# Optimization experiments

Hardware: AMD Instinct MI355X
Metric: run time of the kernel (lower is better)

Reference implementation:

```python
import jax, jax.numpy as jnp
import numpy as np

QUERY_INDS = (0, 1, 2, 3)
HEADS = 8
HEAD_DIM = 64
SCALE = HEAD_DIM ** -0.5
DIM = 512
INNER = HEADS * HEAD_DIM  # 512


def setup_inputs() -> dict:
    key = jax.random.key(0)
    ks = jax.random.split(key, 6)
    B, N = 4, 2048
    x = jax.random.normal(ks[0], (B, N, DIM), dtype=jnp.float32)
    bias = jax.random.normal(ks[1], (B, HEADS, N, N), dtype=jnp.float32)
    # weights stored as (in, out); math-equivalent to torch Linear
    Wq = jax.random.normal(ks[2], (DIM, INNER), dtype=jnp.float32) * (DIM ** -0.5)
    Wkv = jax.random.normal(ks[3], (DIM, 2 * INNER), dtype=jnp.float32) * (DIM ** -0.5)
    Wo = jax.random.normal(ks[4], (INNER, DIM), dtype=jnp.float32) * (INNER ** -0.5)
    bo = jax.random.normal(ks[5], (DIM,), dtype=jnp.float32) * 0.01
    return {"x": x, "bias": bias, "Wq": Wq, "Wkv": Wkv, "Wo": Wo, "bo": bo}


def _split_heads(t):
    # (B, n, H*d) -> (B, H, n, d)
    B, n, _ = t.shape
    return t.reshape(B, n, HEADS, HEAD_DIM).transpose(0, 2, 1, 3)


def reference(x, bias, Wq, Wkv, Wo, bo):
    qi = jnp.array(QUERY_INDS)
    q = _split_heads(x[:, qi] @ Wq)          # (B, H, M, d), M = len(QUERY_INDS)
    kv = x @ Wkv                              # (B, N, 2*inner)
    k, v = jnp.split(kv, 2, axis=-1)
    k = _split_heads(k)                       # (B, H, N, d)
    v = _split_heads(v)                       # (B, H, N, d)
    dots = jnp.einsum('bhmd,bhnd->bhmn', q, k) * SCALE
    dots = dots + bias[:, :, qi]              # gather bias rows at query positions
    attn = jax.nn.softmax(dots, axis=-1)      # dropout=0 (eval)
    out = jnp.einsum('bhmn,bhnd->bhmd', attn, v)
    B, _, M, _ = out.shape
    out = out.transpose(0, 2, 1, 3).reshape(B, M, INNER)  # (B, M, H*d)
    return out @ Wo + bo
```

## Files before the change

### kernel.cpp

```cpp
#include <hip/hip_runtime.h>
#include <stddef.h>

#define B_ 4
#define N_ 2048
#define C_ 512
#define H_ 8
#define D_ 64
#define M_ 4
#define HM_ 32
#define S_ 64
#define SCALE_ 0.125f

#define QK_OFF   0
#define PAX_OFF  65536
#define MLOC_OFF (65536 + 4194304)
#define LLOC_OFF (MLOC_OFF + 8192)
#define QP_OFF   (LLOC_OFF + 8192)
#define OVP_OFF  (QP_OFF + 65536)

__global__ __launch_bounds__(256) void k1a_q(const float* __restrict__ x, const float* __restrict__ Wq,
                                             float* __restrict__ q_part) {
    __shared__ float W[64][68];
    __shared__ float xr[16][68];
    int t = threadIdx.x;
    int c0 = blockIdx.x * 64, j0 = blockIdx.y * 64;
    #pragma unroll
    for (int i = 0; i < 4; i++) {
        int f = t + i * 256; int cc = f >> 4, j4 = f & 15;
        *(float4*)&W[cc][j4 * 4] = *(const float4*)&Wq[(size_t)(c0 + cc) * 512 + j0 + j4 * 4];
    }
    {
        int r = t >> 4, c4 = t & 15;
        int b = r >> 2, m = r & 3;
        *(float4*)&xr[r][c4 * 4] = *(const float4*)&x[((size_t)(b * N_) + m) * C_ + c0 + c4 * 4];
    }
    __syncthreads();
    int j = t & 63, rg = t >> 6;
    float acc[4] = {0, 0, 0, 0};
    #pragma unroll 16
    for (int cc = 0; cc < 64; cc++) {
        float w = W[cc][j];
        #pragma unroll
        for (int i = 0; i < 4; i++) acc[i] += xr[rg * 4 + i][cc] * w;
    }
    #pragma unroll
    for (int i = 0; i < 4; i++) {
        int r = rg * 4 + i;
        q_part[((size_t)blockIdx.x * 16 + r) * 512 + j0 + j] = acc[i];
    }
}

__global__ __launch_bounds__(256) void k1b_qk(const float* __restrict__ Wkv, const float* __restrict__ q_part,
                                              float* __restrict__ qk_ws, float* __restrict__ out) {
    __shared__ float WkT[64][68];
    __shared__ float qh[16][68];
    int t = threadIdx.x;
    int c0 = blockIdx.x * 64; int h = blockIdx.y;
    int bid = blockIdx.y * 8 + blockIdx.x;
    if (bid < 32) out[bid * 256 + t] = 0.f;
    #pragma unroll
    for (int i = 0; i < 4; i++) {
        int f = t + i * 256; int cc = f >> 4, d4 = f & 15;
        float4 v = *(const float4*)&Wkv[(size_t)(c0 + cc) * 1024 + h * 64 + d4 * 4];
        WkT[d4 * 4 + 0][cc] = v.x; WkT[d4 * 4 + 1][cc] = v.y;
        WkT[d4 * 4 + 2][cc] = v.z; WkT[d4 * 4 + 3][cc] = v.w;
    }
    {
        int r = t >> 4, d4 = t & 15;
        float4 a = make_float4(0.f, 0.f, 0.f, 0.f);
        #pragma unroll
        for (int cs = 0; cs < 8; cs++) {
            float4 v = *(const float4*)&q_part[((size_t)cs * 16 + r) * 512 + h * 64 + d4 * 4];
            a.x += v.x; a.y += v.y; a.z += v.z; a.w += v.w;
        }
        *(float4*)&qh[r][d4 * 4] = a;
    }
    __syncthreads();
    int c = t & 63, rg = t >> 6;
    float acc[4] = {0, 0, 0, 0};
    #pragma unroll 16
    for (int d = 0; d < 64; d++) {
        float w = WkT[d][c];
        #pragma unroll
        for (int i = 0; i < 4; i++) acc[i] += qh[rg * 4 + i][d] * w;
    }
    #pragma unroll
    for (int i = 0; i < 4; i++) {
        int r = rg * 4 + i; int b = r >> 2, m = r & 3;
        qk_ws[((size_t)(b * HM_) + h * M_ + m) * 512 + c0 + c] = acc[i] * SCALE_;
    }
}

__global__ __launch_bounds__(256) void k234_flash(const float* __restrict__ x, const float* __restrict__ qk_ws,
                                                  const float* __restrict__ bias,
                                                  float* __restrict__ pax, float* __restrict__ mloc,
                                                  float* __restrict__ lloc) {
    __shared__ __align__(16) float qk_s[32][516];
    __shared__ __align__(16) float scratch[4][32][32];
    __shared__ __align__(16) float dmat[32][36];
    __shared__ __align__(16) float pT[32][36];
    __shared__ float mrow[32];
    __shared__ float red8[32][8];
    int t = threadIdx.x;
    int s = blockIdx.x, b = blockIdx.y;
    int n0 = s * 32;

    #pragma unroll
    for (int k = 0; k < 16; k++) {
        int idx = t + k * 256;
        int row = idx >> 7, c4 = idx & 127;
        *(float4*)&qk_s[row][c4 * 4] =
            *(const float4*)&qk_ws[((size_t)(b * HM_) + row) * 512 + c4 * 4];
    }
    __syncthreads();

    int hmg = t >> 6;
    int ng  = (t >> 3) & 7;
    int cs  = t & 7;
    float d[8][4];
    #pragma unroll
    for (int i = 0; i < 8; i++)
        #pragma unroll
        for (int jn = 0; jn < 4; jn++) d[i][jn] = 0.f;

    const float* xp = &x[((size_t)(b * N_) + n0 + ng * 4) * C_];
    const float* qrow = &qk_s[hmg * 8][0];
    #pragma unroll 2
    for (int step = 0; step < 16; step++) {
        int cbase = cs * 4 + step * 32;
        float4 xv[4];
        #pragma unroll
        for (int jn = 0; jn < 4; jn++)
            xv[jn] = *(const float4*)&xp[(size_t)jn * C_ + cbase];
        #pragma unroll
        for (int i = 0; i < 8; i++) {
            float4 qv = *(const float4*)&qrow[i * 516 + cbase];
            #pragma unroll
            for (int jn = 0; jn < 4; jn++) {
                d[i][jn] += qv.x * xv[jn].x + qv.y * xv[jn].y + qv.z * xv[jn].z + qv.w * xv[jn].w;
            }
        }
    }
    int pos = hmg * 8 + ng;
    if (cs >= 4) {
        #pragma unroll
        for (int i = 0; i < 8; i++)
            *(float4*)&scratch[cs - 4][pos][i * 4] = make_float4(d[i][0], d[i][1], d[i][2], d[i][3]);
    }
    __syncthreads();
    if (cs < 4) {
        #pragma unroll
        for (int i = 0; i < 8; i++) {
            float4 v = *(float4*)&scratch[cs][pos][i * 4];
            d[i][0] += v.x; d[i][1] += v.y; d[i][2] += v.z; d[i][3] += v.w;
        }
    }
    __syncthreads();
    if (cs == 2 || cs == 3) {
        #pragma unroll
        for (int i = 0; i < 8; i++)
            *(float4*)&scratch[cs - 2][pos][i * 4] = make_float4(d[i][0], d[i][1], d[i][2], d[i][3]);
    }
    __syncthreads();
    if (cs < 2) {
        #pragma unroll
        for (int i = 0; i < 8; i++) {
            float4 v = *(float4*)&scratch[cs][pos][i * 4];
            d[i][0] += v.x; d[i][1] += v.y; d[i][2] += v.z; d[i][3] += v.w;
        }
    }
    __syncthreads();
    if (cs == 1) {
        #pragma unroll
        for (int i = 0; i < 8; i++)
            *(float4*)&scratch[0][pos][i * 4] = make_float4(d[i][0], d[i][1], d[i][2], d[i][3]);
    }
    __syncthreads();
    if (cs == 0) {
        #pragma unroll
        for (int i = 0; i < 8; i++) {
            float4 v = *(float4*)&scratch[0][pos][i * 4];
            *(float4*)&dmat[hmg * 8 + i][ng * 4] =
                make_float4(d[i][0] + v.x, d[i][1] + v.y, d[i][2] + v.z, d[i][3] + v.w);
        }
    }
    __syncthreads();

    int row = t >> 3, j = t & 7;
    int h = row >> 2, m = row & 3;
    float4 dv = *(float4*)&dmat[row][j * 4];
    float4 bv = *(const float4*)&bias[(((size_t)(b * H_) + h) * N_ + m) * N_ + n0 + j * 4];
    float v0 = dv.x + bv.x, v1 = dv.y + bv.y, v2 = dv.z + bv.z, v3 = dv.w + bv.w;
    float pmax = fmaxf(fmaxf(v0, v1), fmaxf(v2, v3));
    red8[row][j] = pmax;
    __syncthreads();
    if (j == 0) {
        float mg = red8[row][0];
        #pragma unroll
        for (int k = 1; k < 8; k++) mg = fmaxf(mg, red8[row][k]);
        mrow[row] = mg;
    }
    __syncthreads();
    float mg = mrow[row];
    float e0 = __expf(v0 - mg), e1 = __expf(v1 - mg), e2 = __expf(v2 - mg), e3 = __expf(v3 - mg);
    red8[row][j] = e0 + e1 + e2 + e3;
    __syncthreads();
    if (j == 0) {
        float ls = red8[row][0];
        #pragma unroll
        for (int k = 1; k < 8; k++) ls += red8[row][k];
        mloc[((size_t)(s * B_) + b) * HM_ + row] = mg;
        lloc[((size_t)(s * B_) + b) * HM_ + row] = ls;
    }
    pT[j * 4 + 0][row] = e0; pT[j * 4 + 1][row] = e1;
    pT[j * 4 + 2][row] = e2; pT[j * 4 + 3][row] = e3;
    __syncthreads();

    int cg = t & 63, hw = t >> 6;
    float o[8][8];
    #pragma unroll
    for (int i = 0; i < 8; i++)
        #pragma unroll
        for (int jj = 0; jj < 8; jj++) o[i][jj] = 0.f;
    const float* xb = &x[((size_t)(b * N_) + n0) * C_];
    #pragma unroll 4
    for (int n = 0; n < 32; n++) {
        float4 pa = *(float4*)&pT[n][hw * 8];
        float4 pb = *(float4*)&pT[n][hw * 8 + 4];
        float4 xa = *(const float4*)&xb[(size_t)n * C_ + cg * 4];
        float4 xc = *(const float4*)&xb[(size_t)n * C_ + 256 + cg * 4];
        float pv[8] = {pa.x, pa.y, pa.z, pa.w, pb.x, pb.y, pb.z, pb.w};
        #pragma unroll
        for (int i = 0; i < 8; i++) {
            o[i][0] += pv[i] * xa.x; o[i][1] += pv[i] * xa.y;
            o[i][2] += pv[i] * xa.z; o[i][3] += pv[i] * xa.w;
            o[i][4] += pv[i] * xc.x; o[i][5] += pv[i] * xc.y;
            o[i][6] += pv[i] * xc.z; o[i][7] += pv[i] * xc.w;
        }
    }
    #pragma unroll
    for (int i = 0; i < 8; i++) {
        int hm = hw * 8 + i;
        float* dst = &pax[(((size_t)(s * B_) + b) * HM_ + hm) * 512];
        *(float4*)&dst[cg * 4]       = make_float4(o[i][0], o[i][1], o[i][2], o[i][3]);
        *(float4*)&dst[256 + cg * 4] = make_float4(o[i][4], o[i][5], o[i][6], o[i][7]);
    }
}

__global__ __launch_bounds__(256) void k5a_ov(const float* __restrict__ Wkv, const float* __restrict__ pax,
                                              const float* __restrict__ mloc, const float* __restrict__ lloc,
                                              float* __restrict__ ov_part) {
    __shared__ float Wv[64][68];
    __shared__ float axh[16][68];
    __shared__ float sc[64][16];
    __shared__ float redm[16][16];
    __shared__ float mgl[16], lgl[16];
    int t = threadIdx.x;
    int c0 = blockIdx.x * 64; int h = blockIdx.y;
    #pragma unroll
    for (int i = 0; i < 4; i++) {
        int f = t + i * 256; int cc = f >> 4, e4 = f & 15;
        *(float4*)&Wv[cc][e4 * 4] =
            *(const float4*)&Wkv[(size_t)(c0 + cc) * 1024 + 512 + h * 64 + e4 * 4];
    }
    int r = t & 15, sg = t >> 4;
    int b = r >> 2, m = r & 3;
    float pm = -1e30f;
    #pragma unroll
    for (int k = 0; k < 4; k++) {
        int s = sg * 4 + k;
        pm = fmaxf(pm, mloc[((size_t)(s * B_) + b) * HM_ + h * M_ + m]);
    }
    redm[sg][r] = pm;
    __syncthreads();
    if (t < 16) {
        float mg = redm[0][t];
        #pragma unroll
        for (int k = 1; k < 16; k++) mg = fmaxf(mg, redm[k][t]);
        mgl[t] = mg;
    }
    __syncthreads();
    float mg = mgl[r];
    float pl = 0.f;
    #pragma unroll
    for (int k = 0; k < 4; k++) {
        int s = sg * 4 + k;
        float w = __expf(mloc[((size_t)(s * B_) + b) * HM_ + h * M_ + m] - mg);
        sc[s][r] = w;
        pl += w * lloc[((size_t)(s * B_) + b) * HM_ + h * M_ + m];
    }
    redm[sg][r] = pl;
    __syncthreads();
    if (t < 16) {
        float l = redm[0][t];
        #pragma unroll
        for (int k = 1; k < 16; k++) l += redm[k][t];
        lgl[t] = 1.0f / l;
    }
    __syncthreads();
    float inv = lgl[r];
    #pragma unroll
    for (int k = 0; k < 4; k++) sc[sg * 4 + k][r] *= inv;
    __syncthreads();
    {
        int rr = t >> 4, c4 = t & 15;
        int bb = rr >> 2, mm = rr & 3;
        float4 a = make_float4(0.f, 0.f, 0.f, 0.f);
        for (int s = 0; s < 64; s++) {
            float w = sc[s][rr];
            float4 v = *(const float4*)&pax[(((size_t)(s * B_) + bb) * HM_ + h * M_ + mm) * 512 + c0 + c4 * 4];
            a.x += w * v.x; a.y += w * v.y; a.z += w * v.z; a.w += w * v.w;
        }
        *(float4*)&axh[rr][c4 * 4] = a;
    }
    __syncthreads();
    int e = t & 63, rg = t >> 6;
    float acc[4] = {0, 0, 0, 0};
    #pragma unroll 16
    for (int cc = 0; cc < 64; cc++) {
        float w = Wv[cc][e];
        #pragma unroll
        for (int i = 0; i < 4; i++) acc[i] += axh[rg * 4 + i][cc] * w;
    }
    #pragma unroll
    for (int i = 0; i < 4; i++) {
        int rr = rg * 4 + i;
        ov_part[((size_t)blockIdx.x * 16 + rr) * 512 + h * 64 + e] = acc[i];
    }
}

__global__ __launch_bounds__(256) void k5b_out(const float* __restrict__ Wo, const float* __restrict__ bo,
                                               const float* __restrict__ ov_part, float* __restrict__ out) {
    __shared__ float W[64][68];
    __shared__ float ovr[16][68];
    int t = threadIdx.x;
    int i0 = blockIdx.x * 64; int j0 = blockIdx.y * 64;
    #pragma unroll
    for (int i = 0; i < 4; i++) {
        int f = t + i * 256; int ii = f >> 4, j4 = f & 15;
        *(float4*)&W[ii][j4 * 4] = *(const float4*)&Wo[(size_t)(i0 + ii) * 512 + j0 + j4 * 4];
    }
    {
        int r = t >> 4, c4 = t & 15;
        float4 a = make_float4(0.f, 0.f, 0.f, 0.f);
        #pragma unroll
        for (int cs = 0; cs < 8; cs++) {
            float4 v = *(const float4*)&ov_part[((size_t)cs * 16 + r) * 512 + i0 + c4 * 4];
            a.x += v.x; a.y += v.y; a.z += v.z; a.w += v.w;
        }
        *(float4*)&ovr[r][c4 * 4] = a;
    }
    __syncthreads();
    int j = t & 63, rg = t >> 6;
    float binit = (blockIdx.x == 0) ? bo[j0 + j] : 0.f;
    float acc[4] = {binit, binit, binit, binit};
    #pragma unroll 16
    for (int ii = 0; ii < 64; ii++) {
        float w = W[ii][j];
        #pragma unroll
        for (int i = 0; i < 4; i++) acc[i] += ovr[rg * 4 + i][ii] * w;
    }
    #pragma unroll
    for (int i = 0; i < 4; i++) {
        int r = rg * 4 + i;
        atomicAdd(&out[r * 512 + j0 + j], acc[i]);
    }
}

extern "C" void kernel_launch(void* const* d_in, const int* in_sizes, int n_in,
                              void* d_out, int out_size, void* d_ws, size_t ws_size,
                              hipStream_t stream) {
    const float* x    = (const float*)d_in[0];
    const float* bias = (const float*)d_in[1];
    const float* Wq   = (const float*)d_in[2];
    const float* Wkv  = (const float*)d_in[3];
    const float* Wo   = (const float*)d_in[4];
    const float* bo   = (const float*)d_in[5];
    float* out = (float*)d_out;
    float* ws  = (float*)d_ws;

    float* qk_ws   = ws + QK_OFF;
    float* pax     = ws + PAX_OFF;
    float* mloc    = ws + MLOC_OFF;
    float* lloc    = ws + LLOC_OFF;
    float* q_part  = ws + QP_OFF;
    float* ov_part = ws + OVP_OFF;

    k1a_q<<<dim3(8, 8), 256, 0, stream>>>(x, Wq, q_part);
    k1b_qk<<<dim3(8, 8), 256, 0, stream>>>(Wkv, q_part, qk_ws, out);
    k234_flash<<<dim3(S_, B_), 256, 0, stream>>>(x, qk_ws, bias, pax, mloc, lloc);
    k5a_ov<<<dim3(8, 8), 256, 0, stream>>>(Wkv, pax, mloc, lloc, ov_part);
    k5b_out<<<dim3(8, 8), 256, 0, stream>>>(Wo, bo, ov_part, out);
}
```

Baseline: 610.1 us.

## Fuse five attention kernels into one cooperative kernel with grid syncs

Replaces the five separate launches (Q projection, QK fold, flash partials, OV combine, output projection) with a single cooperative kernel of 256 blocks. Stages are separated by grid-wide barriers, and shared memory is a union of the per-stage layouts. This removes per-launch overhead and inter-kernel gaps. In exchange, all 256 blocks must be co-resident, and in most stages only 64 blocks do work while the rest wait at the barriers.

```diff
diff --git a/kernel.cpp b/kernel.cpp
--- a/kernel.cpp
+++ b/kernel.cpp
@@ -1,5 +1,8 @@
 #include <hip/hip_runtime.h>
+#include <hip/hip_cooperative_groups.h>
 #include <stddef.h>
+
+namespace cg = cooperative_groups;
 
 #define B_ 4
 #define N_ 2048
@@ -18,358 +21,379 @@
 #define QP_OFF   (LLOC_OFF + 8192)
 #define OVP_OFF  (QP_OFF + 65536)
 
-__global__ __launch_bounds__(256) void k1a_q(const float* __restrict__ x, const float* __restrict__ Wq,
-                                             float* __restrict__ q_part) {
-    __shared__ float W[64][68];
-    __shared__ float xr[16][68];
-    int t = threadIdx.x;
-    int c0 = blockIdx.x * 64, j0 = blockIdx.y * 64;
-    #pragma unroll
-    for (int i = 0; i < 4; i++) {
-        int f = t + i * 256; int cc = f >> 4, j4 = f & 15;
-        *(float4*)&W[cc][j4 * 4] = *(const float4*)&Wq[(size_t)(c0 + cc) * 512 + j0 + j4 * 4];
+struct SmemGemm {
+    float W[64][68];
+    float xr[16][68];
+};
+struct SmemFlash {
+    float qk_s[32][516];
+    float scratch[4][32][32];
+    float dmat[32][36];
+    float pT[32][36];
+    float mrow[32];
+    float red8[32][8];
+};
+struct SmemOV {
+    float Wv[64][68];
+    float axh[16][68];
+    float sc[64][16];
+    float redm[16][16];
+    float mgl[16];
+    float lgl[16];
+};
+union __align__(16) SmemAll {
+    SmemGemm g;
+    SmemFlash f;
+    SmemOV o;
+};
+
+__global__ __launch_bounds__(256) void fused_attn(
+        const float* __restrict__ x, const float* __restrict__ bias,
+        const float* __restrict__ Wq, const float* __restrict__ Wkv,
+        const float* __restrict__ Wo, const float* __restrict__ bo,
+        float* __restrict__ out, float* __restrict__ ws) {
+    cg::grid_group gridg = cg::this_grid();
+    __shared__ SmemAll sm;
+
+    float* qk_ws   = ws + QK_OFF;
+    float* pax     = ws + PAX_OFF;
+    float* mloc    = ws + MLOC_OFF;
+    float* lloc    = ws + LLOC_OFF;
+    float* q_part  = ws + QP_OFF;
+    float* ov_part = ws + OVP_OFF;
+
+    const int t = threadIdx.x;
+    const int bid = blockIdx.x;
+
+    if (bid < 64) {
+        int c0 = (bid & 7) * 64, j0 = (bid >> 3) * 64;
+        #pragma unroll
+        for (int i = 0; i < 4; i++) {
+            int f = t + i * 256; int cc = f >> 4, j4 = f & 15;
+            *(float4*)&sm.g.W[cc][j4 * 4] = *(const float4*)&Wq[(size_t)(c0 + cc) * 512 + j0 + j4 * 4];
+        }
+        {
+            int r = t >> 4, c4 = t & 15;
+            int b = r >> 2, m = r & 3;
+            *(float4*)&sm.g.xr[r][c4 * 4] = *(const float4*)&x[((size_t)(b * N_) + m) * C_ + c0 + c4 * 4];
+        }
+        __syncthreads();
+        int j = t & 63, rg = t >> 6;
+        float acc[4] = {0, 0, 0, 0};
+        #pragma unroll 16
+        for (int cc = 0; cc < 64; cc++) {
+            float w = sm.g.W[cc][j];
+            #pragma unroll
+            for (int i = 0; i < 4; i++) acc[i] += sm.g.xr[rg * 4 + i][cc] * w;
+        }
+        #pragma unroll
+        for (int i = 0; i < 4; i++) {
+            int r = rg * 4 + i;
+            q_part[((size_t)(bid & 7) * 16 + r) * 512 + j0 + j] = acc[i];
+        }
+    } else if (bid < 96) {
+        out[(bid - 64) * 256 + t] = 0.f;
     }
+    gridg.sync();
+
+    if (bid < 64) {
+        int c0 = (bid & 7) * 64; int h = bid >> 3;
+        #pragma unroll
+        for (int i = 0; i < 4; i++) {
+            int f = t + i * 256; int cc = f >> 4, d4 = f & 15;
+            float4 v = *(const float4*)&Wkv[(size_t)(c0 + cc) * 1024 + h * 64 + d4 * 4];
+            sm.g.W[d4 * 4 + 0][cc] = v.x; sm.g.W[d4 * 4 + 1][cc] = v.y;
+            sm.g.W[d4 * 4 + 2][cc] = v.z; sm.g.W[d4 * 4 + 3][cc] = v.w;
+        }
+        {
+            int r = t >> 4, d4 = t & 15;
+            float4 a = make_float4(0.f, 0.f, 0.f, 0.f);
+            #pragma unroll
+            for (int cs = 0; cs < 8; cs++) {
+                float4 v = *(const float4*)&q_part[((size_t)cs * 16 + r) * 512 + h * 64 + d4 * 4];
+                a.x += v.x; a.y += v.y; a.z += v.z; a.w += v.w;
+            }
+            *(float4*)&sm.g.xr[r][d4 * 4] = a;
+        }
+        __syncthreads();
+        int c = t & 63, rg = t >> 6;
+        float acc[4] = {0, 0, 0, 0};
+        #pragma unroll 16
+        for (int d = 0; d < 64; d++) {
+            float w = sm.g.W[d][c];
+            #pragma unroll
+            for (int i = 0; i < 4; i++) acc[i] += sm.g.xr[rg * 4 + i][d] * w;
+        }
+        #pragma unroll
+        for (int i = 0; i < 4; i++) {
+            int r = rg * 4 + i; int b = r >> 2, m = r & 3;
+            qk_ws[((size_t)(b * HM_) + h * M_ + m) * 512 + c0 + c] = acc[i] * SCALE_;
+        }
+    }
+    gridg.sync();
+
     {
-        int r = t >> 4, c4 = t & 15;
+        int s = bid & 63, b = bid >> 6;
+        int n0 = s * 32;
+
+        #pragma unroll
+        for (int k = 0; k < 16; k++) {
+            int idx = t + k * 256;
+            int row = idx >> 7, c4 = idx & 127;
+            *(float4*)&sm.f.qk_s[row][c4 * 4] =
+                *(const float4*)&qk_ws[((size_t)(b * HM_) + row) * 512 + c4 * 4];
+        }
+        __syncthreads();
+
+        int hmg = t >> 6;
+        int ng  = (t >> 3) & 7;
+        int cs  = t & 7;
+        float d[8][4];
+        #pragma unroll
+        for (int i = 0; i < 8; i++)
+            #pragma unroll
+            for (int jn = 0; jn < 4; jn++) d[i][jn] = 0.f;
+
+        const float* xp = &x[((size_t)(b * N_) + n0 + ng * 4) * C_];
+        const float* qrow = &sm.f.qk_s[hmg * 8][0];
+        #pragma unroll 2
+        for (int step = 0; step < 16; step++) {
+            int cbase = cs * 4 + step * 32;
+            float4 xv[4];
+            #pragma unroll
+            for (int jn = 0; jn < 4; jn++)
+                xv[jn] = *(const float4*)&xp[(size_t)jn * C_ + cbase];
+            #pragma unroll
+            for (int i = 0; i < 8; i++) {
+                float4 qv = *(const float4*)&qrow[i * 516 + cbase];
+                #pragma unroll
+                for (int jn = 0; jn < 4; jn++) {
+                    d[i][jn] += qv.x * xv[jn].x + qv.y * xv[jn].y + qv.z * xv[jn].z + qv.w * xv[jn].w;
+                }
+            }
+        }
+        int pos = hmg * 8 + ng;
+        if (cs >= 4) {
+            #pragma unroll
+            for (int i = 0; i < 8; i++)
+                *(float4*)&sm.f.scratch[cs - 4][pos][i * 4] = make_float4(d[i][0], d[i][1], d[i][2], d[i][3]);
+        }
+        __syncthreads();
+        if (cs < 4) {
+            #pragma unroll
+            for (int i = 0; i < 8; i++) {
+                float4 v = *(float4*)&sm.f.scratch[cs][pos][i * 4];
+                d[i][0] += v.x; d[i][1] += v.y; d[i][2] += v.z; d[i][3] += v.w;
+            }
+        }
+        __syncthreads();
+        if (cs == 2 || cs == 3) {
+            #pragma unroll
+            for (int i = 0; i < 8; i++)
+                *(float4*)&sm.f.scratch[cs - 2][pos][i * 4] = make_float4(d[i][0], d[i][1], d[i][2], d[i][3]);
+        }
+        __syncthreads();
+        if (cs < 2) {
+            #pragma unroll
+            for (int i = 0; i < 8; i++) {
+                float4 v = *(float4*)&sm.f.scratch[cs][pos][i * 4];
+                d[i][0] += v.x; d[i][1] += v.y; d[i][2] += v.z; d[i][3] += v.w;
+            }
+        }
+        __syncthreads();
+        if (cs == 1) {
+            #pragma unroll
+            for (int i = 0; i < 8; i++)
+                *(float4*)&sm.f.scratch[0][pos][i * 4] = make_float4(d[i][0], d[i][1], d[i][2], d[i][3]);
+        }
+        __syncthreads();
+        if (cs == 0) {
+            #pragma unroll
+            for (int i = 0; i < 8; i++) {
+                float4 v = *(float4*)&sm.f.scratch[0][pos][i * 4];
+                *(float4*)&sm.f.dmat[hmg * 8 + i][ng * 4] =
+                    make_float4(d[i][0] + v.x, d[i][1] + v.y, d[i][2] + v.z, d[i][3] + v.w);
+            }
+        }
+        __syncthreads();
+
+        int row = t >> 3, j = t & 7;
+        int h = row >> 2, m = row & 3;
+        float4 dv = *(float4*)&sm.f.dmat[row][j * 4];
+        float4 bv = *(const float4*)&bias[(((size_t)(b * H_) + h) * N_ + m) * N_ + n0 + j * 4];
+        float v0 = dv.x + bv.x, v1 = dv.y + bv.y, v2 = dv.z + bv.z, v3 = dv.w + bv.w;
+        float pmax = fmaxf(fmaxf(v0, v1), fmaxf(v2, v3));
+        sm.f.red8[row][j] = pmax;
+        __syncthreads();
+        if (j == 0) {
+            float mg = sm.f.red8[row][0];
+            #pragma unroll
+            for (int k = 1; k < 8; k++) mg = fmaxf(mg, sm.f.red8[row][k]);
+            sm.f.mrow[row] = mg;
+        }
+        __syncthreads();
+        float mg = sm.f.mrow[row];
+        float e0 = __expf(v0 - mg), e1 = __expf(v1 - mg), e2 = __expf(v2 - mg), e3 = __expf(v3 - mg);
+        sm.f.red8[row][j] = e0 + e1 + e2 + e3;
+        __syncthreads();
+        if (j == 0) {
+            float ls = sm.f.red8[row][0];
+            #pragma unroll
+            for (int k = 1; k < 8; k++) ls += sm.f.red8[row][k];
+            mloc[((size_t)(s * B_) + b) * HM_ + row] = mg;
+            lloc[((size_t)(s * B_) + b) * HM_ + row] = ls;
+        }
+        sm.f.pT[j * 4 + 0][row] = e0; sm.f.pT[j * 4 + 1][row] = e1;
+        sm.f.pT[j * 4 + 2][row] = e2; sm.f.pT[j * 4 + 3][row] = e3;
+        __syncthreads();
+
+        int cg = t & 63, hw = t >> 6;
+        float o[8][8];
+        #pragma unroll
+        for (int i = 0; i < 8; i++)
+            #pragma unroll
+            for (int jj = 0; jj < 8; jj++) o[i][jj] = 0.f;
+        const float* xb = &x[((size_t)(b * N_) + n0) * C_];
+        #pragma unroll 4
+        for (int n = 0; n < 32; n++) {
+            float4 pa = *(float4*)&sm.f.pT[n][hw * 8];
+            float4 pb = *(float4*)&sm.f.pT[n][hw * 8 + 4];
+            float4 xa = *(const float4*)&xb[(size_t)n * C_ + cg * 4];
+            float4 xc = *(const float4*)&xb[(size_t)n * C_ + 256 + cg * 4];
+            float pv[8] = {pa.x, pa.y, pa.z, pa.w, pb.x, pb.y, pb.z, pb.w};
+            #pragma unroll
+            for (int i = 0; i < 8; i++) {
+                o[i][0] += pv[i] * xa.x; o[i][1] += pv[i] * xa.y;
+                o[i][2] += pv[i] * xa.z; o[i][3] += pv[i] * xa.w;
+                o[i][4] += pv[i] * xc.x; o[i][5] += pv[i] * xc.y;
+                o[i][6] += pv[i] * xc.z; o[i][7] += pv[i] * xc.w;
+            }
+        }
+        #pragma unroll
+        for (int i = 0; i < 8; i++) {
+            int hm = hw * 8 + i;
+            float* dst = &pax[(((size_t)(s * B_) + b) * HM_ + hm) * 512];
+            *(float4*)&dst[cg * 4]       = make_float4(o[i][0], o[i][1], o[i][2], o[i][3]);
+            *(float4*)&dst[256 + cg * 4] = make_float4(o[i][4], o[i][5], o[i][6], o[i][7]);
+        }
+    }
+    gridg.sync();
+
+    if (bid < 64) {
+        int c0 = (bid & 7) * 64; int h = bid >> 3;
+        #pragma unroll
+        for (int i = 0; i < 4; i++) {
+            int f = t + i * 256; int cc = f >> 4, e4 = f & 15;
+            *(float4*)&sm.o.Wv[cc][e4 * 4] =
+                *(const float4*)&Wkv[(size_t)(c0 + cc) * 1024 + 512 + h * 64 + e4 * 4];
+        }
+        int r = t & 15, sg = t >> 4;
         int b = r >> 2, m = r & 3;
-        *(float4*)&xr[r][c4 * 4] = *(const float4*)&x[((size_t)(b * N_) + m) * C_ + c0 + c4 * 4];
+        float pm = -1e30f;
+        #pragma unroll
+        for (int k = 0; k < 4; k++) {
+            int s = sg * 4 + k;
+            pm = fmaxf(pm, mloc[((size_t)(s * B_) + b) * HM_ + h * M_ + m]);
+        }
+        sm.o.redm[sg][r] = pm;
+        __syncthreads();
+        if (t < 16) {
+            float mgv = sm.o.redm[0][t];
+            #pragma unroll
+            for (int k = 1; k < 16; k++) mgv = fmaxf(mgv, sm.o.redm[k][t]);
+            sm.o.mgl[t] = mgv;
+        }
+        __syncthreads();
+        float mgv = sm.o.mgl[r];
+        float pl = 0.f;
+        #pragma unroll
+        for (int k = 0; k < 4; k++) {
+            int s = sg * 4 + k;
+            float w = __expf(mloc[((size_t)(s * B_) + b) * HM_ + h * M_ + m] - mgv);
+            sm.o.sc[s][r] = w;
+            pl += w * lloc[((size_t)(s * B_) + b) * HM_ + h * M_ + m];
+        }
+        sm.o.redm[sg][r] = pl;
+        __syncthreads();
+        if (t < 16) {
+            float l = sm.o.redm[0][t];
+            #pragma unroll
+            for (int k = 1; k < 16; k++) l += sm.o.redm[k][t];
+            sm.o.lgl[t] = 1.0f / l;
+        }
+        __syncthreads();
+        float inv = sm.o.lgl[r];
+        #pragma unroll
+        for (int k = 0; k < 4; k++) sm.o.sc[sg * 4 + k][r] *= inv;
+        __syncthreads();
+        {
+            int rr = t >> 4, c4 = t & 15;
+            int bb = rr >> 2, mm = rr & 3;
+            float4 a = make_float4(0.f, 0.f, 0.f, 0.f);
+            #pragma unroll 8
+            for (int s = 0; s < 64; s++) {
+                float w = sm.o.sc[s][rr];
+                float4 v = *(const float4*)&pax[(((size_t)(s * B_) + bb) * HM_ + h * M_ + mm) * 512 + c0 + c4 * 4];
+                a.x += w * v.x; a.y += w * v.y; a.z += w * v.z; a.w += w * v.w;
+            }
+            *(float4*)&sm.o.axh[rr][c4 * 4] = a;
+        }
+        __syncthreads();
+        int e = t & 63, rg = t >> 6;
+        float acc[4] = {0, 0, 0, 0};
+        #pragma unroll 16
+        for (int cc = 0; cc < 64; cc++) {
+            float w = sm.o.Wv[cc][e];
+            #pragma unroll
+            for (int i = 0; i < 4; i++) acc[i] += sm.o.axh[rg * 4 + i][cc] * w;
+        }
+        #pragma unroll
+        for (int i = 0; i < 4; i++) {
+            int rr = rg * 4 + i;
+            ov_part[((size_t)(bid & 7) * 16 + rr) * 512 + h * 64 + e] = acc[i];
+        }
     }
-    __syncthreads();
-    int j = t & 63, rg = t >> 6;
-    float acc[4] = {0, 0, 0, 0};
-    #pragma unroll 16
-    for (int cc = 0; cc < 64; cc++) {
-        float w = W[cc][j];
-        #pragma unroll
-        for (int i = 0; i < 4; i++) acc[i] += xr[rg * 4 + i][cc] * w;
-    }
-    #pragma unroll
-    for (int i = 0; i < 4; i++) {
-        int r = rg * 4 + i;
-        q_part[((size_t)blockIdx.x * 16 + r) * 512 + j0 + j] = acc[i];
-    }
-}
-
-__global__ __launch_bounds__(256) void k1b_qk(const float* __restrict__ Wkv, const float* __restrict__ q_part,
-                                              float* __restrict__ qk_ws, float* __restrict__ out) {
-    __shared__ float WkT[64][68];
-    __shared__ float qh[16][68];
-    int t = threadIdx.x;
-    int c0 = blockIdx.x * 64; int h = blockIdx.y;
-    int bid = blockIdx.y * 8 + blockIdx.x;
-    if (bid < 32) out[bid * 256 + t] = 0.f;
-    #pragma unroll
-    for (int i = 0; i < 4; i++) {
-        int f = t + i * 256; int cc = f >> 4, d4 = f & 15;
-        float4 v = *(const float4*)&Wkv[(size_t)(c0 + cc) * 1024 + h * 64 + d4 * 4];
-        WkT[d4 * 4 + 0][cc] = v.x; WkT[d4 * 4 + 1][cc] = v.y;
-        WkT[d4 * 4 + 2][cc] = v.z; WkT[d4 * 4 + 3][cc] = v.w;
-    }
-    {
-        int r = t >> 4, d4 = t & 15;
-        float4 a = make_float4(0.f, 0.f, 0.f, 0.f);
-        #pragma unroll
-        for (int cs = 0; cs < 8; cs++) {
-            float4 v = *(const float4*)&q_part[((size_t)cs * 16 + r) * 512 + h * 64 + d4 * 4];
-            a.x += v.x; a.y += v.y; a.z += v.z; a.w += v.w;
-        }
-        *(float4*)&qh[r][d4 * 4] = a;
-    }
-    __syncthreads();
-    int c = t & 63, rg = t >> 6;
-    float acc[4] = {0, 0, 0, 0};
-    #pragma unroll 16
-    for (int d = 0; d < 64; d++) {
-        float w = WkT[d][c];
-        #pragma unroll
-        for (int i = 0; i < 4; i++) acc[i] += qh[rg * 4 + i][d] * w;
-    }
-    #pragma unroll
-    for (int i = 0; i < 4; i++) {
-        int r = rg * 4 + i; int b = r >> 2, m = r & 3;
-        qk_ws[((size_t)(b * HM_) + h * M_ + m) * 512 + c0 + c] = acc[i] * SCALE_;
-    }
-}
-
-__global__ __launch_bounds__(256) void k234_flash(const float* __restrict__ x, const float* __restrict__ qk_ws,
-                                                  const float* __restrict__ bias,
-                                                  float* __restrict__ pax, float* __restrict__ mloc,
-                                                  float* __restrict__ lloc) {
-    __shared__ __align__(16) float qk_s[32][516];
-    __shared__ __align__(16) float scratch[4][32][32];
-    __shared__ __align__(16) float dmat[32][36];
-    __shared__ __align__(16) float pT[32][36];
-    __shared__ float mrow[32];
-    __shared__ float red8[32][8];
-    int t = threadIdx.x;
-    int s = blockIdx.x, b = blockIdx.y;
-    int n0 = s * 32;
-
-    #pragma unroll
-    for (int k = 0; k < 16; k++) {
-        int idx = t + k * 256;
-        int row = idx >> 7, c4 = idx & 127;
-        *(float4*)&qk_s[row][c4 * 4] =
-            *(const float4*)&qk_ws[((size_t)(b * HM_) + row) * 512 + c4 * 4];
-    }
-    __syncthreads();
-
-    int hmg = t >> 6;
-    int ng  = (t >> 3) & 7;
-    int cs  = t & 7;
-    float d[8][4];
-    #pragma unroll
-    for (int i = 0; i < 8; i++)
-        #pragma unroll
-        for (int jn = 0; jn < 4; jn++) d[i][jn] = 0.f;
-
-    const float* xp = &x[((size_t)(b * N_) + n0 + ng * 4) * C_];
-    const float* qrow = &qk_s[hmg * 8][0];
-    #pragma unroll 2
-    for (int step = 0; step < 16; step++) {
-        int cbase = cs * 4 + step * 32;
-        float4 xv[4];
-        #pragma unroll
-        for (int jn = 0; jn < 4; jn++)
-            xv[jn] = *(const float4*)&xp[(size_t)jn * C_ + cbase];
-        #pragma unroll
-        for (int i = 0; i < 8; i++) {
-            float4 qv = *(const float4*)&qrow[i * 516 + cbase];
-            #pragma unroll
-            for (int jn = 0; jn < 4; jn++) {
-                d[i][jn] += qv.x * xv[jn].x + qv.y * xv[jn].y + qv.z * xv[jn].z + qv.w * xv[jn].w;
-            }
-        }
-    }
-    int pos = hmg * 8 + ng;
-    if (cs >= 4) {
-        #pragma unroll
-        for (int i = 0; i < 8; i++)
-            *(float4*)&scratch[cs - 4][pos][i * 4] = make_float4(d[i][0], d[i][1], d[i][2], d[i][3]);
-    }
-    __syncthreads();
-    if (cs < 4) {
-        #pragma unroll
-        for (int i = 0; i < 8; i++) {
-            float4 v = *(float4*)&scratch[cs][pos][i * 4];
-            d[i][0] += v.x; d[i][1] += v.y; d[i][2] += v.z; d[i][3] += v.w;
-        }
-    }
-    __syncthreads();
-    if (cs == 2 || cs == 3) {
-        #pragma unroll
-        for (int i = 0; i < 8; i++)
-            *(float4*)&scratch[cs - 2][pos][i * 4] = make_float4(d[i][0], d[i][1], d[i][2], d[i][3]);
-    }
-    __syncthreads();
-    if (cs < 2) {
-        #pragma unroll
-        for (int i = 0; i < 8; i++) {
-            float4 v = *(float4*)&scratch[cs][pos][i * 4];
-            d[i][0] += v.x; d[i][1] += v.y; d[i][2] += v.z; d[i][3] += v.w;
-        }
-    }
-    __syncthreads();
-    if (cs == 1) {
-        #pragma unroll
-        for (int i = 0; i < 8; i++)
-            *(float4*)&scratch[0][pos][i * 4] = make_float4(d[i][0], d[i][1], d[i][2], d[i][3]);
-    }
-    __syncthreads();
-    if (cs == 0) {
-        #pragma unroll
-        for (int i = 0; i < 8; i++) {
-            float4 v = *(float4*)&scratch[0][pos][i * 4];
-            *(float4*)&dmat[hmg * 8 + i][ng * 4] =
-                make_float4(d[i][0] + v.x, d[i][1] + v.y, d[i][2] + v.z, d[i][3] + v.w);
-        }
-    }
-    __syncthreads();
-
-    int row = t >> 3, j = t & 7;
-    int h = row >> 2, m = row & 3;
-    float4 dv = *(float4*)&dmat[row][j * 4];
-    float4 bv = *(const float4*)&bias[(((size_t)(b * H_) + h) * N_ + m) * N_ + n0 + j * 4];
-    float v0 = dv.x + bv.x, v1 = dv.y + bv.y, v2 = dv.z + bv.z, v3 = dv.w + bv.w;
-    float pmax = fmaxf(fmaxf(v0, v1), fmaxf(v2, v3));
-    red8[row][j] = pmax;
-    __syncthreads();
-    if (j == 0) {
-        float mg = red8[row][0];
-        #pragma unroll
-        for (int k = 1; k < 8; k++) mg = fmaxf(mg, red8[row][k]);
-        mrow[row] = mg;
-    }
-    __syncthreads();
-    float mg = mrow[row];
-    float e0 = __expf(v0 - mg), e1 = __expf(v1 - mg), e2 = __expf(v2 - mg), e3 = __expf(v3 - mg);
-    red8[row][j] = e0 + e1 + e2 + e3;
-    __syncthreads();
-    if (j == 0) {
-        float ls = red8[row][0];
-        #pragma unroll
-        for (int k = 1; k < 8; k++) ls += red8[row][k];
-        mloc[((size_t)(s * B_) + b) * HM_ + row] = mg;
-        lloc[((size_t)(s * B_) + b) * HM_ + row] = ls;
-    }
-    pT[j * 4 + 0][row] = e0; pT[j * 4 + 1][row] = e1;
-    pT[j * 4 + 2][row] = e2; pT[j * 4 + 3][row] = e3;
-    __syncthreads();
-
-    int cg = t & 63, hw = t >> 6;
-    float o[8][8];
-    #pragma unroll
-    for (int i = 0; i < 8; i++)
-        #pragma unroll
-        for (int jj = 0; jj < 8; jj++) o[i][jj] = 0.f;
-    const float* xb = &x[((size_t)(b * N_) + n0) * C_];
-    #pragma unroll 4
-    for (int n = 0; n < 32; n++) {
-        float4 pa = *(float4*)&pT[n][hw * 8];
-        float4 pb = *(float4*)&pT[n][hw * 8 + 4];
-        float4 xa = *(const float4*)&xb[(size_t)n * C_ + cg * 4];
-        float4 xc = *(const float4*)&xb[(size_t)n * C_ + 256 + cg * 4];
-        float pv[8] = {pa.x, pa.y, pa.z, pa.w, pb.x, pb.y, pb.z, pb.w};
-        #pragma unroll
-        for (int i = 0; i < 8; i++) {
-            o[i][0] += pv[i] * xa.x; o[i][1] += pv[i] * xa.y;
-            o[i][2] += pv[i] * xa.z; o[i][3] += pv[i] * xa.w;
-            o[i][4] += pv[i] * xc.x; o[i][5] += pv[i] * xc.y;
-            o[i][6] += pv[i] * xc.z; o[i][7] += pv[i] * xc.w;
-        }
-    }
-    #pragma unroll
-    for (int i = 0; i < 8; i++) {
-        int hm = hw * 8 + i;
-        float* dst = &pax[(((size_t)(s * B_) + b) * HM_ + hm) * 512];
-        *(float4*)&dst[cg * 4]       = make_float4(o[i][0], o[i][1], o[i][2], o[i][3]);
-        *(float4*)&dst[256 + cg * 4] = make_float4(o[i][4], o[i][5], o[i][6], o[i][7]);
-    }
-}
-
-__global__ __launch_bounds__(256) void k5a_ov(const float* __restrict__ Wkv, const float* __restrict__ pax,
-                                              const float* __restrict__ mloc, const float* __restrict__ lloc,
-                                              float* __restrict__ ov_part) {
-    __shared__ float Wv[64][68];
-    __shared__ float axh[16][68];
-    __shared__ float sc[64][16];
-    __shared__ float redm[16][16];
-    __shared__ float mgl[16], lgl[16];
-    int t = threadIdx.x;
-    int c0 = blockIdx.x * 64; int h = blockIdx.y;
-    #pragma unroll
-    for (int i = 0; i < 4; i++) {
-        int f = t + i * 256; int cc = f >> 4, e4 = f & 15;
-        *(float4*)&Wv[cc][e4 * 4] =
-            *(const float4*)&Wkv[(size_t)(c0 + cc) * 1024 + 512 + h * 64 + e4 * 4];
-    }
-    int r = t & 15, sg = t >> 4;
-    int b = r >> 2, m = r & 3;
-    float pm = -1e30f;
-    #pragma unroll
-    for (int k = 0; k < 4; k++) {
-        int s = sg * 4 + k;
-        pm = fmaxf(pm, mloc[((size_t)(s * B_) + b) * HM_ + h * M_ + m]);
-    }
-    redm[sg][r] = pm;
-    __syncthreads();
-    if (t < 16) {
-        float mg = redm[0][t];
-        #pragma unroll
-        for (int k = 1; k < 16; k++) mg = fmaxf(mg, redm[k][t]);
-        mgl[t] = mg;
-    }
-    __syncthreads();
-    float mg = mgl[r];
-    float pl = 0.f;
-    #pragma unroll
-    for (int k = 0; k < 4; k++) {
-        int s = sg * 4 + k;
-        float w = __expf(mloc[((size_t)(s * B_) + b) * HM_ + h * M_ + m] - mg);
-        sc[s][r] = w;
-        pl += w * lloc[((size_t)(s * B_) + b) * HM_ + h * M_ + m];
-    }
-    redm[sg][r] = pl;
-    __syncthreads();
-    if (t < 16) {
-        float l = redm[0][t];
-        #pragma unroll
-        for (int k = 1; k < 16; k++) l += redm[k][t];
-        lgl[t] = 1.0f / l;
-    }
-    __syncthreads();
-    float inv = lgl[r];
-    #pragma unroll
-    for (int k = 0; k < 4; k++) sc[sg * 4 + k][r] *= inv;
-    __syncthreads();
-    {
-        int rr = t >> 4, c4 = t & 15;
-        int bb = rr >> 2, mm = rr & 3;
-        float4 a = make_float4(0.f, 0.f, 0.f, 0.f);
-        for (int s = 0; s < 64; s++) {
-            float w = sc[s][rr];
-            float4 v = *(const float4*)&pax[(((size_t)(s * B_) + bb) * HM_ + h * M_ + mm) * 512 + c0 + c4 * 4];
-            a.x += w * v.x; a.y += w * v.y; a.z += w * v.z; a.w += w * v.w;
-        }
-        *(float4*)&axh[rr][c4 * 4] = a;
-    }
-    __syncthreads();
-    int e = t & 63, rg = t >> 6;
-    float acc[4] = {0, 0, 0, 0};
-    #pragma unroll 16
-    for (int cc = 0; cc < 64; cc++) {
-        float w = Wv[cc][e];
-        #pragma unroll
-        for (int i = 0; i < 4; i++) acc[i] += axh[rg * 4 + i][cc] * w;
-    }
-    #pragma unroll
-    for (int i = 0; i < 4; i++) {
-        int rr = rg * 4 + i;
-        ov_part[((size_t)blockIdx.x * 16 + rr) * 512 + h * 64 + e] = acc[i];
-    }
-}
-
-__global__ __launch_bounds__(256) void k5b_out(const float* __restrict__ Wo, const float* __restrict__ bo,
-                                               const float* __restrict__ ov_part, float* __restrict__ out) {
-    __shared__ float W[64][68];
-    __shared__ float ovr[16][68];
-    int t = threadIdx.x;
-    int i0 = blockIdx.x * 64; int j0 = blockIdx.y * 64;
-    #pragma unroll
-    for (int i = 0; i < 4; i++) {
-        int f = t + i * 256; int ii = f >> 4, j4 = f & 15;
-        *(float4*)&W[ii][j4 * 4] = *(const float4*)&Wo[(size_t)(i0 + ii) * 512 + j0 + j4 * 4];
-    }
-    {
-        int r = t >> 4, c4 = t & 15;
-        float4 a = make_float4(0.f, 0.f, 0.f, 0.f);
-        #pragma unroll
-        for (int cs = 0; cs < 8; cs++) {
-            float4 v = *(const float4*)&ov_part[((size_t)cs * 16 + r) * 512 + i0 + c4 * 4];
-            a.x += v.x; a.y += v.y; a.z += v.z; a.w += v.w;
-        }
-        *(float4*)&ovr[r][c4 * 4] = a;
-    }
-    __syncthreads();
-    int j = t & 63, rg = t >> 6;
-    float binit = (blockIdx.x == 0) ? bo[j0 + j] : 0.f;
-    float acc[4] = {binit, binit, binit, binit};
-    #pragma unroll 16
-    for (int ii = 0; ii < 64; ii++) {
-        float w = W[ii][j];
-        #pragma unroll
-        for (int i = 0; i < 4; i++) acc[i] += ovr[rg * 4 + i][ii] * w;
-    }
-    #pragma unroll
-    for (int i = 0; i < 4; i++) {
-        int r = rg * 4 + i;
-        atomicAdd(&out[r * 512 + j0 + j], acc[i]);
+    gridg.sync();
+
+    if (bid < 64) {
+        int i0 = (bid & 7) * 64; int j0 = (bid >> 3) * 64;
+        #pragma unroll
+        for (int i = 0; i < 4; i++) {
+            int f = t + i * 256; int ii = f >> 4, j4 = f & 15;
+            *(float4*)&sm.g.W[ii][j4 * 4] = *(const float4*)&Wo[(size_t)(i0 + ii) * 512 + j0 + j4 * 4];
+        }
+        {
+            int r = t >> 4, c4 = t & 15;
+            float4 a = make_float4(0.f, 0.f, 0.f, 0.f);
+            #pragma unroll
+            for (int cs = 0; cs < 8; cs++) {
+                float4 v = *(const float4*)&ov_part[((size_t)cs * 16 + r) * 512 + i0 + c4 * 4];
+                a.x += v.x; a.y += v.y; a.z += v.z; a.w += v.w;
+            }
+            *(float4*)&sm.g.xr[r][c4 * 4] = a;
+        }
+        __syncthreads();
+        int j = t & 63, rg = t >> 6;
+        float binit = ((bid & 7) == 0) ? bo[j0 + j] : 0.f;
+        float acc[4] = {binit, binit, binit, binit};
+        #pragma unroll 16
+        for (int ii = 0; ii < 64; ii++) {
+            float w = sm.g.W[ii][j];
+            #pragma unroll
+            for (int i = 0; i < 4; i++) acc[i] += sm.g.xr[rg * 4 + i][ii] * w;
+        }
+        #pragma unroll
+        for (int i = 0; i < 4; i++) {
+            int r = rg * 4 + i;
+            atomicAdd(&out[r * 512 + j0 + j], acc[i]);
+        }
     }
 }
 
 extern "C" void kernel_launch(void* const* d_in, const int* in_sizes, int n_in,
                               void* d_out, int out_size, void* d_ws, size_t ws_size,
                               hipStream_t stream) {
+    (void)in_sizes; (void)n_in; (void)out_size; (void)ws_size;
     const float* x    = (const float*)d_in[0];
     const float* bias = (const float*)d_in[1];
     const float* Wq   = (const float*)d_in[2];
@@ -379,16 +403,6 @@
     float* out = (float*)d_out;
     float* ws  = (float*)d_ws;
 
-    float* qk_ws   = ws + QK_OFF;
-    float* pax     = ws + PAX_OFF;
-    float* mloc    = ws + MLOC_OFF;
-    float* lloc    = ws + LLOC_OFF;
-    float* q_part  = ws + QP_OFF;
-    float* ov_part = ws + OVP_OFF;
-
-    k1a_q<<<dim3(8, 8), 256, 0, stream>>>(x, Wq, q_part);
-    k1b_qk<<<dim3(8, 8), 256, 0, stream>>>(Wkv, q_part, qk_ws, out);
-    k234_flash<<<dim3(S_, B_), 256, 0, stream>>>(x, qk_ws, bias, pax, mloc, lloc);
-    k5a_ov<<<dim3(8, 8), 256, 0, stream>>>(Wkv, pax, mloc, lloc, ov_part);
-    k5b_out<<<dim3(8, 8), 256, 0, stream>>>(Wo, bo, ov_part, out);
+    void* args[8] = {&x, &bias, &Wq, &Wkv, &Wo, &bo, &out, &ws};
+    hipLaunchCooperativeKernel((void*)fused_attn, dim3(256), dim3(256), args, 0, stream);
 }
```

Result: slower. 745.4 us (+22.2%).
